# Kernel optimization log

Measured on AMD Instinct MI355X. Metric: run time of the kernel, lower is better.

The kernel has to match this reference:

```python
import jax, jax.numpy as jnp
import numpy as np

NUM_USERS = 100000
NUM_ITEMS = 100000
N = NUM_USERS + NUM_ITEMS
D = 64
E = 1200000


def setup_inputs() -> dict:
    key = jax.random.key(0)
    k1, k2, k3, k4, k5 = jax.random.split(key, 5)
    edge_index = jax.random.randint(k1, (2, E), 0, N, dtype=jnp.int64)
    user_emb = jax.random.normal(k2, (NUM_USERS, D), dtype=jnp.float32)
    item_emb = jax.random.normal(k3, (NUM_ITEMS, D), dtype=jnp.float32)
    W1 = jax.random.normal(k4, (D, D), dtype=jnp.float32) / np.sqrt(D)
    b1 = jnp.zeros((D,), dtype=jnp.float32)
    W2 = jax.random.normal(k5, (D, D), dtype=jnp.float32) / np.sqrt(D)
    b2 = jnp.zeros((D,), dtype=jnp.float32)
    return {"edge_index": edge_index, "user_emb": user_emb, "item_emb": item_emb,
            "W1": W1, "b1": b1, "W2": W2, "b2": b2}


def _gcn_conv(x, row, col, norm, W, b, n_nodes):
    # x: [N, D]; row/col: [E+N] (with self-loops); norm: [E+N]
    x = x @ W                                  # linear transform (no bias in lin)
    msg = x[row] * norm[:, None]               # gather + scale (memory-bound)
    out = jax.ops.segment_sum(msg, col, num_segments=n_nodes)  # scatter-add
    return out + b


def reference(edge_index, user_emb, item_emb, W1, b1, W2, b2):
    x = jnp.concatenate([user_emb, item_emb], axis=0)  # [N, D]
    n_nodes = x.shape[0]
    # gcn_norm: add self-loops, symmetric deg^{-1/2} normalization
    sl = jnp.arange(n_nodes, dtype=edge_index.dtype)
    row = jnp.concatenate([edge_index[0], sl])
    col = jnp.concatenate([edge_index[1], sl])
    deg = jax.ops.segment_sum(jnp.ones_like(col, dtype=x.dtype), col,
                              num_segments=n_nodes)
    dinv = jnp.where(deg > 0, jax.lax.rsqrt(jnp.maximum(deg, 1e-12)), 0.0)
    norm = dinv[row] * dinv[col]
    x = _gcn_conv(x, row, col, norm, W1, b1, n_nodes)
    x = _gcn_conv(x, row, col, norm, W2, b2, n_nodes)
    return x
```

## Files before the change

kernel.cpp:

```cpp
#include <hip/hip_runtime.h>

#define DIM 64
#define GPW 4
#define BSHIFT 9
#define BSPAN 512
#define MAXNB 512
#define CNTB 256

typedef __attribute__((ext_vector_type(8))) __bf16 bf16x8;
typedef __attribute__((ext_vector_type(8))) unsigned short u16x8;
typedef __attribute__((ext_vector_type(4))) float f32x4;

__device__ __forceinline__ f32x4 mfma16(bf16x8 a, bf16x8 b, f32x4 c) {
    return __builtin_amdgcn_mfma_f32_16x16x32_bf16(a, b, c, 0, 0, 0);
}

__device__ __forceinline__ float bf2f(unsigned short u) {
    return __uint_as_float((unsigned)u << 16);
}


__device__ __forceinline__ void gemm_f32_body(
    int bid, const float* __restrict__ xa_, const float* __restrict__ xb_,
    int split, const float* __restrict__ W, const float* __restrict__ dinv,
    __bf16* __restrict__ h, int n, int ngroups) {
    int lane = threadIdx.x & 63;
    int q = lane >> 4, t = lane & 15;
    int wv = __builtin_amdgcn_readfirstlane((threadIdx.x >> 6) & 3);
    int g0 = (bid * 4 + wv) * GPW;
    if (g0 >= ngroups) return;

    bf16x8 Bf[4][2];
#pragma unroll
    for (int nt = 0; nt < 4; ++nt)
#pragma unroll
        for (int kt = 0; kt < 2; ++kt) {
            bf16x8 f;
#pragma unroll
            for (int j = 0; j < 8; ++j)
                f[j] = (__bf16)W[(kt * 32 + q * 8 + j) * DIM + nt * 16 + t];
            Bf[nt][kt] = f;
        }

    auto loadA = [&](int r0, f32x4* raw) {
        int row = r0 + t;
        if (row >= n) row = n - 1;
        const float* xr = (row < split)
            ? (xa_ + (size_t)row * DIM)
            : (xb_ + (size_t)(row - split) * DIM);
        raw[0] = *(const f32x4*)(xr + q * 8);
        raw[1] = *(const f32x4*)(xr + q * 8 + 4);
        raw[2] = *(const f32x4*)(xr + 32 + q * 8);
        raw[3] = *(const f32x4*)(xr + 32 + q * 8 + 4);
    };

    f32x4 cur[4];
    loadA(g0 * 16, cur);

#pragma unroll 1
    for (int gi = 0; gi < GPW; ++gi) {
        int g = g0 + gi;
        if (g >= ngroups) break;
        int r0 = g * 16;
        f32x4 nxt[4];
        bool pf = (gi + 1 < GPW) && (g + 1 < ngroups);
        if (pf) loadA(r0 + 16, nxt);

        bf16x8 A0, A1;
#pragma unroll
        for (int j = 0; j < 4; ++j) {
            A0[j] = (__bf16)cur[0][j]; A0[j + 4] = (__bf16)cur[1][j];
            A1[j] = (__bf16)cur[2][j]; A1[j + 4] = (__bf16)cur[3][j];
        }

        f32x4 z = {0.f, 0.f, 0.f, 0.f};
        f32x4 acc[4];
#pragma unroll
        for (int nt = 0; nt < 4; ++nt)
            acc[nt] = mfma16(A1, Bf[nt][1], mfma16(A0, Bf[nt][0], z));

#pragma unroll
        for (int nt = 0; nt < 4; ++nt)
#pragma unroll
            for (int reg = 0; reg < 4; ++reg) {
                int row = r0 + q * 4 + reg;
                if (row < n)
                    h[(size_t)row * DIM + nt * 16 + t] = (__bf16)acc[nt][reg];
            }
#pragma unroll
        for (int i = 0; i < 4; ++i) cur[i] = nxt[i];
    }
}


__global__ __launch_bounds__(256) void count_gemm_kernel(
    const int* __restrict__ ei, int* __restrict__ bpart, int E_,
    const float* __restrict__ ua, const float* __restrict__ ub, int split,
    const float* __restrict__ W1, __bf16* __restrict__ h, int n, int ngroups) {
    if (blockIdx.x >= CNTB) {
        gemm_f32_body(blockIdx.x - CNTB, ua, ub, split, W1, nullptr, h, n, ngroups);
        return;
    }
    __shared__ int hist[MAXNB];
    int tid = threadIdx.x;
    int bid = blockIdx.x;
    hist[tid] = 0; hist[tid + 256] = 0;
    __syncthreads();
    int chunk = (E_ + CNTB - 1) / CNTB;
    int e0 = bid * chunk, e1 = min(E_, e0 + chunk);
    for (int e = e0 + tid; e < e1; e += 256)
        atomicAdd(&hist[ei[E_ + e] >> BSHIFT], 1);
    __syncthreads();
    bpart[bid * MAXNB + tid] = hist[tid];
    bpart[bid * MAXNB + tid + 256] = hist[tid + 256];
}

__global__ __launch_bounds__(512) void bucket_scan_kernel(
    const int* __restrict__ bpart, int* __restrict__ bptr,
    int* __restrict__ bcur, int* __restrict__ rowptr,
    int nblk, int N_, int E_) {
    __shared__ int sm[512];
    int tid = threadIdx.x;
    int tot = 0;
#pragma unroll 8
    for (int blk = 0; blk < nblk; ++blk)
        tot += bpart[blk * MAXNB + tid];
    sm[tid] = tot;
    __syncthreads();
    for (int off = 1; off < 512; off <<= 1) {
        int t = 0;
        if (tid >= off) t = sm[tid - off];
        __syncthreads();
        if (tid >= off) sm[tid] += t;
        __syncthreads();
    }
    int ex = sm[tid] - tot;
    bptr[tid] = ex;
    bcur[tid] = ex;
    if (tid == 0) { bptr[MAXNB] = E_; rowptr[N_] = E_; }
}

__global__ __launch_bounds__(512) void scatter_kernel(
    const int* __restrict__ ei, int* __restrict__ bcur,
    unsigned* __restrict__ packed, int E_, int nblk) {
    __shared__ int h[MAXNB];
    int tid = threadIdx.x;
    int chunk = (E_ + nblk - 1) / nblk;
    int e0 = blockIdx.x * chunk, e1 = min(E_, e0 + chunk);
    h[tid] = 0;
    __syncthreads();
    for (int e = e0 + tid; e < e1; e += 512)
        atomicAdd(&h[ei[E_ + e] >> BSHIFT], 1);
    __syncthreads();
    int c = h[tid];
    h[tid] = c ? atomicAdd(&bcur[tid], c) : 0;
    __syncthreads();
    for (int e = e0 + tid; e < e1; e += 512) {
        int s = ei[e], d = ei[E_ + e];
        int b = d >> BSHIFT;
        int pos = atomicAdd(&h[b], 1);
        packed[pos] = ((unsigned)s << BSHIFT) | (unsigned)(d & (BSPAN - 1));
    }
}

__global__ __launch_bounds__(256) void bucket_sort_kernel(
    const unsigned* __restrict__ packed, const int* __restrict__ bptr,
    int* __restrict__ rowptr, int* __restrict__ srcs,
    float* __restrict__ dinv, int N_) {
    __shared__ int cnt[BSPAN];
    __shared__ int sc[256];
    int tid = threadIdx.x;
    int b = blockIdx.x;
    int beg = bptr[b], end = bptr[b + 1];
    int node0 = b << BSHIFT;
    int nn = min(BSPAN, N_ - node0);
    cnt[tid] = 0; cnt[tid + 256] = 0;
    __syncthreads();
    for (int i = beg + tid; i < end; i += 256)
        atomicAdd(&cnt[packed[i] & (BSPAN - 1)], 1);
    __syncthreads();
    int degA = cnt[tid], degB = cnt[tid + 256];
    int a0 = cnt[2 * tid], a1 = cnt[2 * tid + 1];
    if (tid < nn) dinv[node0 + tid] = rsqrtf((float)(1 + degA));
    if (tid + 256 < nn) dinv[node0 + tid + 256] = rsqrtf((float)(1 + degB));
    int tot = a0 + a1;
    sc[tid] = tot;
    __syncthreads();
    for (int off = 1; off < 256; off <<= 1) {
        int t = 0;
        if (tid >= off) t = sc[tid - off];
        __syncthreads();
        if (tid >= off) sc[tid] += t;
        __syncthreads();
    }
    int ex = sc[tid] - tot;
    cnt[2 * tid] = ex;
    cnt[2 * tid + 1] = ex + a0;
    __syncthreads();
    if (tid < nn) rowptr[node0 + tid] = beg + cnt[tid];
    if (tid + 256 < nn) rowptr[node0 + tid + 256] = beg + cnt[tid + 256];
    __syncthreads();
    for (int i = beg + tid; i < end; i += 256) {
        unsigned p = packed[i];
        int pos = atomicAdd(&cnt[p & (BSPAN - 1)], 1);
        srcs[beg + pos] = (int)(p >> BSHIFT);
    }
}


__global__ __launch_bounds__(256) void gemm_bf16_kernel(
    const __bf16* __restrict__ x, const float* __restrict__ W,
    const float* __restrict__ dinv, __bf16* __restrict__ h, int n, int ngroups) {
    int lane = threadIdx.x & 63;
    int q = lane >> 4, t = lane & 15;
    int wv = __builtin_amdgcn_readfirstlane(threadIdx.x >> 6);
    int g0 = (blockIdx.x * 4 + wv) * GPW;
    if (g0 >= ngroups) return;

    bf16x8 Bf[4][2];
#pragma unroll
    for (int nt = 0; nt < 4; ++nt)
#pragma unroll
        for (int kt = 0; kt < 2; ++kt) {
            bf16x8 f;
#pragma unroll
            for (int j = 0; j < 8; ++j)
                f[j] = (__bf16)W[(kt * 32 + q * 8 + j) * DIM + nt * 16 + t];
            Bf[nt][kt] = f;
        }

    auto loadA = [&](int r0, f32x4* raw) {
        int row = r0 + t;
        if (row >= n) row = n - 1;
        const __bf16* xr = x + (size_t)row * DIM;
        raw[0] = *(const f32x4*)(xr + q * 8);
        raw[1] = *(const f32x4*)(xr + 32 + q * 8);
    };

    f32x4 cur[2];
    loadA(g0 * 16, cur);

#pragma unroll 1
    for (int gi = 0; gi < GPW; ++gi) {
        int g = g0 + gi;
        if (g >= ngroups) break;
        int r0 = g * 16;
        f32x4 nxt[2];
        bool pf = (gi + 1 < GPW) && (g + 1 < ngroups);
        if (pf) loadA(r0 + 16, nxt);

        bf16x8 A0 = __builtin_bit_cast(bf16x8, cur[0]);
        bf16x8 A1 = __builtin_bit_cast(bf16x8, cur[1]);

        f32x4 z = {0.f, 0.f, 0.f, 0.f};
        f32x4 acc[4];
#pragma unroll
        for (int nt = 0; nt < 4; ++nt)
            acc[nt] = mfma16(A1, Bf[nt][1], mfma16(A0, Bf[nt][0], z));

        f32x4 d4 = *(const f32x4*)(dinv + r0 + q * 4);
#pragma unroll
        for (int nt = 0; nt < 4; ++nt)
#pragma unroll
            for (int reg = 0; reg < 4; ++reg) {
                int row = r0 + q * 4 + reg;
                if (row < n)
                    h[(size_t)row * DIM + nt * 16 + t] =
                        (__bf16)(acc[nt][reg] * d4[reg]);
            }
        cur[0] = nxt[0]; cur[1] = nxt[1];
    }
}

template <typename OutT, bool SRC_SCALE>
__global__ __launch_bounds__(256) void agg_kernel(
    const int* __restrict__ rowptr, const int* __restrict__ srcs,
    const __bf16* __restrict__ h, const float* __restrict__ bias,
    const float* __restrict__ dinv, OutT* __restrict__ out, int n) {
    int lane = threadIdx.x & 63;
    int t8 = lane & 7;
    int wv = threadIdx.x >> 6;
    int node = (blockIdx.x * 4 + wv) * 8 + (lane >> 3);
    bool alive = node < n;
    int nd = alive ? node : (n - 1);
    int beg = rowptr[nd], end = rowptr[nd + 1];
    float dn = dinv[nd];

    u16x8 sv = *(const u16x8*)(h + (size_t)nd * DIM + t8 * 8);
    float selfscale = SRC_SCALE ? dn : 1.f;
    float acc[8];
#pragma unroll
    for (int j = 0; j < 8; ++j) acc[j] = bf2f(sv[j]) * selfscale;

    int i = beg;
    while (i < end) {
        int idx = i + t8;
        int sl = (idx < end) ? srcs[idx] : 0;
        float dsl = 0.f;
        if (SRC_SCALE && idx < end) dsl = dinv[sl];
        u16x8 vv[8];
#pragma unroll
        for (int k = 0; k < 8; ++k) {
            int s = __shfl(sl, (lane & 56) | k);
            vv[k] = *(const u16x8*)(h + (size_t)s * DIM + t8 * 8);
        }
#pragma unroll
        for (int k = 0; k < 8; ++k)
            if (i + k < end) {
                float w = SRC_SCALE ? __shfl(dsl, (lane & 56) | k) : 1.f;
#pragma unroll
                for (int j = 0; j < 8; ++j)
                    acc[j] = SRC_SCALE ? fmaf(bf2f(vv[k][j]), w, acc[j])
                                       : (acc[j] + bf2f(vv[k][j]));
            }
        i += 8;
    }

    f32x4 b0 = *(const f32x4*)(bias + t8 * 8);
    f32x4 b1 = *(const f32x4*)(bias + t8 * 8 + 4);
    if (alive) {
        if constexpr (sizeof(OutT) == 4) {
            f32x4 o0, o1;
#pragma unroll
            for (int j = 0; j < 4; ++j) {
                o0[j] = fmaf(dn, acc[j],     b0[j]);
                o1[j] = fmaf(dn, acc[j + 4], b1[j]);
            }
            float* op = (float*)out + (size_t)node * DIM + t8 * 8;
            *(f32x4*)op = o0;
            *(f32x4*)(op + 4) = o1;
        } else {
            bf16x8 o;
#pragma unroll
            for (int j = 0; j < 4; ++j) {
                o[j]     = (__bf16)fmaf(dn, acc[j],     b0[j]);
                o[j + 4] = (__bf16)fmaf(dn, acc[j + 4], b1[j]);
            }
            *(bf16x8*)((__bf16*)out + (size_t)node * DIM + t8 * 8) = o;
        }
    }
}

static inline size_t align16(size_t x) { return (x + 15) & ~(size_t)15; }

extern "C" void kernel_launch(void* const* d_in, const int* in_sizes, int n_in,
                              void* d_out, int out_size, void* d_ws, size_t ws_size,
                              hipStream_t stream) {
    const int* ei         = (const int*)d_in[0];
    const float* user_emb = (const float*)d_in[1];
    const float* item_emb = (const float*)d_in[2];
    const float* W1 = (const float*)d_in[3];
    const float* b1 = (const float*)d_in[4];
    const float* W2 = (const float*)d_in[5];
    const float* b2 = (const float*)d_in[6];
    float* out = (float*)d_out;

    const int E_ = in_sizes[0] / 2;
    const int NU = in_sizes[1] / DIM;
    const int NI = in_sizes[2] / DIM;
    const int N_ = NU + NI;
    const int NB = (N_ + BSPAN - 1) >> BSHIFT;

    char* p = (char*)d_ws;
    int* srcs   = (int*)p;               p += align16((size_t)E_ * 4);
    __bf16* h   = (__bf16*)p;            p += align16((size_t)N_ * DIM * 2);
    __bf16* t1  = (__bf16*)p;            p += align16((size_t)N_ * DIM * 2);
    float* dinv = (float*)p;             p += align16((size_t)N_ * 4);
    int* rowptr = (int*)p;               p += align16((size_t)(N_ + 1) * 4);
    int* bpart  = (int*)p;               p += align16((size_t)CNTB * MAXNB * 4);
    int* bptr   = (int*)p;               p += align16((size_t)(MAXNB + 1) * 4);
    int* bcur   = (int*)p;               p += align16((size_t)MAXNB * 4);
    unsigned* packed = (unsigned*)t1;

    int NG = (N_ + 15) / 16;
    int gblocks = (NG + 4 * GPW - 1) / (4 * GPW);
    int ablocks = (N_ + 31) / 32;

    count_gemm_kernel<<<CNTB + gblocks, 256, 0, stream>>>(
        ei, bpart, E_, user_emb, item_emb, NU, W1, h, N_, NG);
    bucket_scan_kernel<<<1, 512, 0, stream>>>(bpart, bptr, bcur, rowptr,
                                              CNTB, N_, E_);
    scatter_kernel<<<CNTB, 512, 0, stream>>>(ei, bcur, packed, E_, CNTB);
    bucket_sort_kernel<<<NB, 256, 0, stream>>>(packed, bptr, rowptr, srcs, dinv, N_);

    agg_kernel<__bf16, true><<<ablocks, 256, 0, stream>>>(rowptr, srcs, h, b1,
                                                          dinv, t1, N_);
    gemm_bf16_kernel<<<gblocks, 256, 0, stream>>>(t1, W2, dinv, h, N_, NG);
    agg_kernel<float, false><<<ablocks, 256, 0, stream>>>(rowptr, srcs, h, b2,
                                                          dinv, out, N_);
}
```

Before: 247.1 us.

## Fuse second-layer GEMM into aggregation by reordering aggregate-then-transform

Layer 2 now aggregates the layer-1 output first, then applies W2 with MFMA inside the same kernel. This uses the linearity of the normalized adjacency and removes the standalone GEMM launch and its write-read of the intermediate features. The cost is that each wave reloads W2 from global memory, and half of each 16-row MFMA tile is wasted because a wave holds only 8 nodes. Source-side dinv scaling is applied in both aggregations.

```diff
diff --git a/kernel.cpp b/kernel.cpp
--- a/kernel.cpp
+++ b/kernel.cpp
@@ -9,6 +9,7 @@
 
 typedef __attribute__((ext_vector_type(8))) __bf16 bf16x8;
 typedef __attribute__((ext_vector_type(8))) unsigned short u16x8;
+typedef __attribute__((ext_vector_type(4))) unsigned u32x4;
 typedef __attribute__((ext_vector_type(4))) float f32x4;
 
 __device__ __forceinline__ f32x4 mfma16(bf16x8 a, bf16x8 b, f32x4 c) {
@@ -22,8 +23,8 @@
 
 __device__ __forceinline__ void gemm_f32_body(
     int bid, const float* __restrict__ xa_, const float* __restrict__ xb_,
-    int split, const float* __restrict__ W, const float* __restrict__ dinv,
-    __bf16* __restrict__ h, int n, int ngroups) {
+    int split, const float* __restrict__ W, __bf16* __restrict__ h,
+    int n, int ngroups) {
     int lane = threadIdx.x & 63;
     int q = lane >> 4, t = lane & 15;
     int wv = __builtin_amdgcn_readfirstlane((threadIdx.x >> 6) & 3);
@@ -98,7 +99,7 @@
     const float* __restrict__ ua, const float* __restrict__ ub, int split,
     const float* __restrict__ W1, __bf16* __restrict__ h, int n, int ngroups) {
     if (blockIdx.x >= CNTB) {
-        gemm_f32_body(blockIdx.x - CNTB, ua, ub, split, W1, nullptr, h, n, ngroups);
+        gemm_f32_body(blockIdx.x - CNTB, ua, ub, split, W1, h, n, ngroups);
         return;
     }
     __shared__ int hist[MAXNB];
@@ -208,75 +209,10 @@
 }
 
 
-__global__ __launch_bounds__(256) void gemm_bf16_kernel(
-    const __bf16* __restrict__ x, const float* __restrict__ W,
-    const float* __restrict__ dinv, __bf16* __restrict__ h, int n, int ngroups) {
-    int lane = threadIdx.x & 63;
-    int q = lane >> 4, t = lane & 15;
-    int wv = __builtin_amdgcn_readfirstlane(threadIdx.x >> 6);
-    int g0 = (blockIdx.x * 4 + wv) * GPW;
-    if (g0 >= ngroups) return;
-
-    bf16x8 Bf[4][2];
-#pragma unroll
-    for (int nt = 0; nt < 4; ++nt)
-#pragma unroll
-        for (int kt = 0; kt < 2; ++kt) {
-            bf16x8 f;
-#pragma unroll
-            for (int j = 0; j < 8; ++j)
-                f[j] = (__bf16)W[(kt * 32 + q * 8 + j) * DIM + nt * 16 + t];
-            Bf[nt][kt] = f;
-        }
-
-    auto loadA = [&](int r0, f32x4* raw) {
-        int row = r0 + t;
-        if (row >= n) row = n - 1;
-        const __bf16* xr = x + (size_t)row * DIM;
-        raw[0] = *(const f32x4*)(xr + q * 8);
-        raw[1] = *(const f32x4*)(xr + 32 + q * 8);
-    };
-
-    f32x4 cur[2];
-    loadA(g0 * 16, cur);
-
-#pragma unroll 1
-    for (int gi = 0; gi < GPW; ++gi) {
-        int g = g0 + gi;
-        if (g >= ngroups) break;
-        int r0 = g * 16;
-        f32x4 nxt[2];
-        bool pf = (gi + 1 < GPW) && (g + 1 < ngroups);
-        if (pf) loadA(r0 + 16, nxt);
-
-        bf16x8 A0 = __builtin_bit_cast(bf16x8, cur[0]);
-        bf16x8 A1 = __builtin_bit_cast(bf16x8, cur[1]);
-
-        f32x4 z = {0.f, 0.f, 0.f, 0.f};
-        f32x4 acc[4];
-#pragma unroll
-        for (int nt = 0; nt < 4; ++nt)
-            acc[nt] = mfma16(A1, Bf[nt][1], mfma16(A0, Bf[nt][0], z));
-
-        f32x4 d4 = *(const f32x4*)(dinv + r0 + q * 4);
-#pragma unroll
-        for (int nt = 0; nt < 4; ++nt)
-#pragma unroll
-            for (int reg = 0; reg < 4; ++reg) {
-                int row = r0 + q * 4 + reg;
-                if (row < n)
-                    h[(size_t)row * DIM + nt * 16 + t] =
-                        (__bf16)(acc[nt][reg] * d4[reg]);
-            }
-        cur[0] = nxt[0]; cur[1] = nxt[1];
-    }
-}
-
-template <typename OutT, bool SRC_SCALE>
-__global__ __launch_bounds__(256) void agg_kernel(
+__global__ __launch_bounds__(256) void agg1_kernel(
     const int* __restrict__ rowptr, const int* __restrict__ srcs,
     const __bf16* __restrict__ h, const float* __restrict__ bias,
-    const float* __restrict__ dinv, OutT* __restrict__ out, int n) {
+    const float* __restrict__ dinv, __bf16* __restrict__ out, int n) {
     int lane = threadIdx.x & 63;
     int t8 = lane & 7;
     int wv = threadIdx.x >> 6;
@@ -287,17 +223,15 @@
     float dn = dinv[nd];
 
     u16x8 sv = *(const u16x8*)(h + (size_t)nd * DIM + t8 * 8);
-    float selfscale = SRC_SCALE ? dn : 1.f;
     float acc[8];
 #pragma unroll
-    for (int j = 0; j < 8; ++j) acc[j] = bf2f(sv[j]) * selfscale;
+    for (int j = 0; j < 8; ++j) acc[j] = bf2f(sv[j]) * dn;
 
     int i = beg;
     while (i < end) {
         int idx = i + t8;
         int sl = (idx < end) ? srcs[idx] : 0;
-        float dsl = 0.f;
-        if (SRC_SCALE && idx < end) dsl = dinv[sl];
+        float dsl = (idx < end) ? dinv[sl] : 0.f;
         u16x8 vv[8];
 #pragma unroll
         for (int k = 0; k < 8; ++k) {
@@ -307,11 +241,10 @@
 #pragma unroll
         for (int k = 0; k < 8; ++k)
             if (i + k < end) {
-                float w = SRC_SCALE ? __shfl(dsl, (lane & 56) | k) : 1.f;
+                float w = __shfl(dsl, (lane & 56) | k);
 #pragma unroll
                 for (int j = 0; j < 8; ++j)
-                    acc[j] = SRC_SCALE ? fmaf(bf2f(vv[k][j]), w, acc[j])
-                                       : (acc[j] + bf2f(vv[k][j]));
+                    acc[j] = fmaf(bf2f(vv[k][j]), w, acc[j]);
             }
         i += 8;
     }
@@ -319,24 +252,102 @@
     f32x4 b0 = *(const f32x4*)(bias + t8 * 8);
     f32x4 b1 = *(const f32x4*)(bias + t8 * 8 + 4);
     if (alive) {
-        if constexpr (sizeof(OutT) == 4) {
-            f32x4 o0, o1;
-#pragma unroll
-            for (int j = 0; j < 4; ++j) {
-                o0[j] = fmaf(dn, acc[j],     b0[j]);
-                o1[j] = fmaf(dn, acc[j + 4], b1[j]);
+        bf16x8 o;
+#pragma unroll
+        for (int j = 0; j < 4; ++j) {
+            o[j]     = (__bf16)fmaf(dn, acc[j],     b0[j]);
+            o[j + 4] = (__bf16)fmaf(dn, acc[j + 4], b1[j]);
+        }
+        *(bf16x8*)(out + (size_t)node * DIM + t8 * 8) = o;
+    }
+}
+
+__global__ __launch_bounds__(256) void agg_gemm2_kernel(
+    const int* __restrict__ rowptr, const int* __restrict__ srcs,
+    const __bf16* __restrict__ t1, const float* __restrict__ W2,
+    const float* __restrict__ b2, const float* __restrict__ dinv,
+    float* __restrict__ out, int n) {
+    int lane = threadIdx.x & 63;
+    int t8 = lane & 7;
+    int wv = __builtin_amdgcn_readfirstlane(threadIdx.x >> 6);
+    int q = lane >> 4, t = lane & 15;
+    int wbase = (blockIdx.x * 4 + wv) * 8;
+    int node = wbase + (lane >> 3);
+    int nd = (node < n) ? node : (n - 1);
+    int beg = rowptr[nd], end = rowptr[nd + 1];
+    float dn = dinv[nd];
+
+    u16x8 sv = *(const u16x8*)(t1 + (size_t)nd * DIM + t8 * 8);
+    float acc[8];
+#pragma unroll
+    for (int j = 0; j < 8; ++j) acc[j] = bf2f(sv[j]) * dn;
+
+    int i = beg;
+    while (i < end) {
+        int idx = i + t8;
+        int sl = (idx < end) ? srcs[idx] : 0;
+        float dsl = (idx < end) ? dinv[sl] : 0.f;
+        u16x8 vv[8];
+#pragma unroll
+        for (int k = 0; k < 8; ++k) {
+            int s = __shfl(sl, (lane & 56) | k);
+            vv[k] = *(const u16x8*)(t1 + (size_t)s * DIM + t8 * 8);
+        }
+#pragma unroll
+        for (int k = 0; k < 8; ++k)
+            if (i + k < end) {
+                float w = __shfl(dsl, (lane & 56) | k);
+#pragma unroll
+                for (int j = 0; j < 8; ++j)
+                    acc[j] = fmaf(bf2f(vv[k][j]), w, acc[j]);
             }
-            float* op = (float*)out + (size_t)node * DIM + t8 * 8;
-            *(f32x4*)op = o0;
-            *(f32x4*)(op + 4) = o1;
-        } else {
-            bf16x8 o;
-#pragma unroll
-            for (int j = 0; j < 4; ++j) {
-                o[j]     = (__bf16)fmaf(dn, acc[j],     b0[j]);
-                o[j + 4] = (__bf16)fmaf(dn, acc[j + 4], b1[j]);
+        i += 8;
+    }
+
+    bf16x8 o;
+#pragma unroll
+    for (int j = 0; j < 8; ++j) o[j] = (__bf16)(dn * acc[j]);
+
+    __builtin_amdgcn_sched_barrier(0);
+    bf16x8 Bf[4][2];
+#pragma unroll
+    for (int nt = 0; nt < 4; ++nt)
+#pragma unroll
+        for (int kt = 0; kt < 2; ++kt) {
+            bf16x8 f;
+#pragma unroll
+            for (int j = 0; j < 8; ++j)
+                f[j] = (__bf16)W2[(kt * 32 + q * 8 + j) * DIM + nt * 16 + t];
+            Bf[nt][kt] = f;
+        }
+
+    u32x4 ov = __builtin_bit_cast(u32x4, o);
+    int s0 = ((t & 7) << 3) | q;
+    u32x4 a0v, a1v;
+#pragma unroll
+    for (int j = 0; j < 4; ++j) {
+        a0v[j] = (unsigned)__shfl((int)ov[j], s0);
+        a1v[j] = (unsigned)__shfl((int)ov[j], s0 + 4);
+    }
+    bf16x8 A0 = __builtin_bit_cast(bf16x8, a0v);
+    bf16x8 A1 = __builtin_bit_cast(bf16x8, a1v);
+
+    f32x4 z = {0.f, 0.f, 0.f, 0.f};
+    f32x4 acc2[4];
+#pragma unroll
+    for (int nt = 0; nt < 4; ++nt)
+        acc2[nt] = mfma16(A1, Bf[nt][1], mfma16(A0, Bf[nt][0], z));
+
+    if (q < 2) {
+#pragma unroll
+        for (int nt = 0; nt < 4; ++nt) {
+            float bv = b2[nt * 16 + t];
+#pragma unroll
+            for (int reg = 0; reg < 4; ++reg) {
+                int row = wbase + q * 4 + reg;
+                if (row < n)
+                    out[(size_t)row * DIM + nt * 16 + t] = acc2[nt][reg] + bv;
             }
-            *(bf16x8*)((__bf16*)out + (size_t)node * DIM + t8 * 8) = o;
         }
     }
 }
@@ -383,9 +394,7 @@
     scatter_kernel<<<CNTB, 512, 0, stream>>>(ei, bcur, packed, E_, CNTB);
     bucket_sort_kernel<<<NB, 256, 0, stream>>>(packed, bptr, rowptr, srcs, dinv, N_);
 
-    agg_kernel<__bf16, true><<<ablocks, 256, 0, stream>>>(rowptr, srcs, h, b1,
-                                                          dinv, t1, N_);
-    gemm_bf16_kernel<<<gblocks, 256, 0, stream>>>(t1, W2, dinv, h, N_, NG);
-    agg_kernel<float, false><<<ablocks, 256, 0, stream>>>(rowptr, srcs, h, b2,
-                                                          dinv, out, N_);
-}
+    agg1_kernel<<<ablocks, 256, 0, stream>>>(rowptr, srcs, h, b1, dinv, t1, N_);
+    agg_gemm2_kernel<<<ablocks, 256, 0, stream>>>(rowptr, srcs, t1, W2, b2,
+                                                  dinv, out, N_);
+}
```

After: 259.2 us. +4.9%, slower.

## Split first-layer GEMM across count, scatter and sort kernels

Applied to the files above, without the earlier changes.

Splits the first-layer feature GEMM blocks into three portions and runs them as extra blocks inside the count, scatter and bucket-sort kernels. Each portion overlaps with the graph-building work, which is memory- and atomic-bound and leaves many compute units underused. In the scatter kernel, each 512-thread block handles two GEMM block ids, one per 256-thread half. The risk is extra contention and uneven load in the scatter and sort phases.

```diff
diff --git a/kernel.cpp b/kernel.cpp
--- a/kernel.cpp
+++ b/kernel.cpp
@@ -19,11 +19,10 @@
     return __uint_as_float((unsigned)u << 16);
 }
 
-
 __device__ __forceinline__ void gemm_f32_body(
     int bid, const float* __restrict__ xa_, const float* __restrict__ xb_,
-    int split, const float* __restrict__ W, const float* __restrict__ dinv,
-    __bf16* __restrict__ h, int n, int ngroups) {
+    int split, const float* __restrict__ W, __bf16* __restrict__ h,
+    int n, int ngroups) {
     int lane = threadIdx.x & 63;
     int q = lane >> 4, t = lane & 15;
     int wv = __builtin_amdgcn_readfirstlane((threadIdx.x >> 6) & 3);
@@ -98,7 +97,7 @@
     const float* __restrict__ ua, const float* __restrict__ ub, int split,
     const float* __restrict__ W1, __bf16* __restrict__ h, int n, int ngroups) {
     if (blockIdx.x >= CNTB) {
-        gemm_f32_body(blockIdx.x - CNTB, ua, ub, split, W1, nullptr, h, n, ngroups);
+        gemm_f32_body(blockIdx.x - CNTB, ua, ub, split, W1, h, n, ngroups);
         return;
     }
     __shared__ int hist[MAXNB];
@@ -140,12 +139,20 @@
     if (tid == 0) { bptr[MAXNB] = E_; rowptr[N_] = E_; }
 }
 
-__global__ __launch_bounds__(512) void scatter_kernel(
+__global__ __launch_bounds__(512) void scatter_gemm_kernel(
     const int* __restrict__ ei, int* __restrict__ bcur,
-    unsigned* __restrict__ packed, int E_, int nblk) {
+    unsigned* __restrict__ packed, int E_,
+    const float* __restrict__ ua, const float* __restrict__ ub, int split,
+    const float* __restrict__ W1, __bf16* __restrict__ hout, int n,
+    int ngroups, int goff) {
+    if (blockIdx.x >= CNTB) {
+        int bid = goff + (blockIdx.x - CNTB) * 2 + (threadIdx.x >> 8);
+        gemm_f32_body(bid, ua, ub, split, W1, hout, n, ngroups);
+        return;
+    }
     __shared__ int h[MAXNB];
     int tid = threadIdx.x;
-    int chunk = (E_ + nblk - 1) / nblk;
+    int chunk = (E_ + CNTB - 1) / CNTB;
     int e0 = blockIdx.x * chunk, e1 = min(E_, e0 + chunk);
     h[tid] = 0;
     __syncthreads();
@@ -163,10 +170,18 @@
     }
 }
 
-__global__ __launch_bounds__(256) void bucket_sort_kernel(
+__global__ __launch_bounds__(256) void sort_gemm_kernel(
     const unsigned* __restrict__ packed, const int* __restrict__ bptr,
     int* __restrict__ rowptr, int* __restrict__ srcs,
-    float* __restrict__ dinv, int N_) {
+    float* __restrict__ dinv, int N_, int NB,
+    const float* __restrict__ ua, const float* __restrict__ ub, int split,
+    const float* __restrict__ W1, __bf16* __restrict__ hout, int n,
+    int ngroups, int goff) {
+    if (blockIdx.x >= NB) {
+        gemm_f32_body(goff + ((int)blockIdx.x - NB), ua, ub, split, W1, hout,
+                      n, ngroups);
+        return;
+    }
     __shared__ int cnt[BSPAN];
     __shared__ int sc[256];
     int tid = threadIdx.x;
@@ -376,12 +391,19 @@
     int gblocks = (NG + 4 * GPW - 1) / (4 * GPW);
     int ablocks = (N_ + 31) / 32;
 
-    count_gemm_kernel<<<CNTB + gblocks, 256, 0, stream>>>(
+    int GC = gblocks / 3;
+    int GB = (gblocks / 3) & ~1;
+    int GA = gblocks - GB - GC;
+
+    count_gemm_kernel<<<CNTB + GA, 256, 0, stream>>>(
         ei, bpart, E_, user_emb, item_emb, NU, W1, h, N_, NG);
     bucket_scan_kernel<<<1, 512, 0, stream>>>(bpart, bptr, bcur, rowptr,
                                               CNTB, N_, E_);
-    scatter_kernel<<<CNTB, 512, 0, stream>>>(ei, bcur, packed, E_, CNTB);
-    bucket_sort_kernel<<<NB, 256, 0, stream>>>(packed, bptr, rowptr, srcs, dinv, N_);
+    scatter_gemm_kernel<<<CNTB + GB / 2, 512, 0, stream>>>(
+        ei, bcur, packed, E_, user_emb, item_emb, NU, W1, h, N_, NG, GA);
+    sort_gemm_kernel<<<NB + GC, 256, 0, stream>>>(
+        packed, bptr, rowptr, srcs, dinv, N_, NB,
+        user_emb, item_emb, NU, W1, h, N_, NG, GA + GB);
 
     agg_kernel<__bf16, true><<<ablocks, 256, 0, stream>>>(rowptr, srcs, h, b1,
                                                           dinv, t1, N_);
```

Result: no change. 246.8 us (-0.1%).
